# Kernel optimization log

Hardware: AMD Instinct MI355X
Metric: run time of the kernel (lower is better)

Reference implementation:

```python
import jax, jax.numpy as jnp
import numpy as np

D_MODEL, D_STATE, D_CONV, D_INNER = 1024, 16, 4, 2048
BATCH, SEQ = 2, 2048


def setup_inputs() -> dict:
    key = jax.random.key(0)
    ks = jax.random.split(key, 12)
    s = 0.02
    inp = {
        "x": jax.random.normal(ks[0], (BATCH, SEQ, D_MODEL), jnp.float32),
        # Linear weights stored (in, out): y = x @ W + b (equivalent to torch x @ W.T + b)
        "W_in": jax.random.normal(ks[1], (D_MODEL, 2 * D_INNER), jnp.float32) * s,
        "b_in": jnp.zeros((2 * D_INNER,), jnp.float32),
        # depthwise conv kernel (OIH) with groups=d_inner -> (d_inner, 1, d_conv)
        "conv_w": jax.random.normal(ks[2], (D_INNER, 1, D_CONV), jnp.float32) * s,
        "conv_b": jnp.zeros((D_INNER,), jnp.float32),
        "W_x": jax.random.normal(ks[3], (D_INNER, 2 * D_STATE), jnp.float32) * s,
        "b_x": jnp.zeros((2 * D_STATE,), jnp.float32),
        "W_dt": jax.random.normal(ks[4], (D_INNER, D_INNER), jnp.float32) * s,
        "b_dt": jnp.zeros((D_INNER,), jnp.float32),
        # A_log init: log(arange(1..d_state)) tiled over d_inner, as in the module
        "A_log": jnp.log(jnp.tile(jnp.arange(1, D_STATE + 1, dtype=jnp.float32), (D_INNER, 1))),
        "D": jnp.ones((D_INNER,), jnp.float32),
        "W_out": jax.random.normal(ks[5], (D_INNER, D_MODEL), jnp.float32) * s,
        "b_out": jnp.zeros((D_MODEL,), jnp.float32),
    }
    return inp


def reference(x, W_in, b_in, conv_w, conv_b, W_x, b_x, W_dt, b_dt, A_log, D, W_out, b_out):
    d_inner, d_state = A_log.shape
    d_conv = conv_w.shape[-1]
    bsz, seq_len, _ = x.shape

    xz = x @ W_in + b_in                      # (B, L, 2*Din)
    xh, z = jnp.split(xz, 2, axis=-1)

    # causal depthwise conv: torch pads both sides by d_conv-1 then slices [:L]
    # == left-pad-only causal conv
    xc = jnp.transpose(xh, (0, 2, 1))         # (B, Din, L)
    xc = jax.lax.conv_general_dilated(
        xc, conv_w, window_strides=(1,), padding=[(d_conv - 1, 0)],
        dimension_numbers=("NCH", "OIH", "NCH"), feature_group_count=d_inner)
    xc = xc + conv_b[None, :, None]
    xh = jax.nn.silu(jnp.transpose(xc, (0, 2, 1)))  # (B, L, Din)

    A = -jnp.exp(A_log)                       # (Din, N)
    x_dbl = xh @ W_x + b_x                    # (B, L, 2N)
    Bmat = x_dbl[..., d_state:]               # second chunk; first chunk is discarded
    delta = jax.nn.softplus(xh @ W_dt + b_dt) # (B, L, Din)

    def step(h, inp):
        d_t, b_t, u_t = inp                    # (B,Din), (B,N), (B,Din)
        dA = jnp.exp(d_t[:, :, None] * A)      # (B, Din, N)
        dBu = d_t[:, :, None] * b_t[:, None, :] * u_t[:, :, None]
        h = dA * h + dBu
        return h, h.sum(-1)                    # y_t: (B, Din)

    h0 = jnp.zeros((bsz, d_inner, d_state), x.dtype)
    _, ys = jax.lax.scan(step, h0, (jnp.swapaxes(delta, 0, 1),
                                    jnp.swapaxes(Bmat, 0, 1),
                                    jnp.swapaxes(xh, 0, 1)))
    y = jnp.swapaxes(ys, 0, 1) + xh * D       # skip connection with D
    y = y * jax.nn.silu(z)                    # gate
    return y @ W_out + b_out                  # (B, L, d_model)
```

## Files before the change

### kernel.cpp

```cpp
#include <hip/hip_runtime.h>
#include <stdint.h>

#define NDM   1024
#define NDS   16
#define NDC   4
#define NDI   2048
#define NB    2
#define NL    2048
#define MROWS (NB*NL)
#define CCH   32
#define CLEN  64

typedef __bf16 bf16x8 __attribute__((ext_vector_type(8)));
typedef float  f32x4  __attribute__((ext_vector_type(4)));
typedef short  short8 __attribute__((ext_vector_type(8)));

__device__ __forceinline__ short f2bf(float f) {
  union { float f; unsigned u; } x; x.f = f;
  unsigned r = (x.u + 0x7FFFu + ((x.u >> 16) & 1u)) >> 16;
  return (short)r;
}

__device__ __forceinline__ void gload16(const void* g, void* l) {
  __builtin_amdgcn_global_load_lds(
      (__attribute__((address_space(1))) void*)(uintptr_t)g,
      (__attribute__((address_space(3))) void*)l,
      16, 0, 0);
}

__device__ __forceinline__ size_t fgoff(int row, int k8, int K) {
  return (size_t)(row >> 4) * K * 16 + (size_t)k8 * 128 + (row & 15) * 8;
}

__global__ __launch_bounds__(256) void cvt_fg_kernel(
    const float* __restrict__ in, short* __restrict__ out) {
  __shared__ short slab[16][1032];
  const int tid = threadIdx.x;
  const int g = blockIdx.x;
  const float* p = in + (size_t)g * 16 * 1024;
  #pragma unroll
  for (int u = 0; u < 8; ++u) {
    int unit = u * 256 + tid;
    int rr = unit >> 7, cc = unit & 127;
    const float* rp = p + (size_t)rr * 1024 + cc * 8;
    #pragma unroll
    for (int e = 0; e < 8; ++e) slab[rr][cc * 8 + e] = f2bf(rp[e]);
  }
  __syncthreads();
  short* op = out + (size_t)g * 16384;
  #pragma unroll
  for (int u = 0; u < 8; ++u) {
    int u2 = u * 256 + tid;
    int rr = u2 & 15, k8 = u2 >> 4;
    *(short8*)&op[k8 * 128 + rr * 8] = *(short8*)&slab[rr][k8 * 8];
  }
}

__global__ __launch_bounds__(256) void transpose_fg_kernel(
    const float* __restrict__ in, short* __restrict__ out, int K, int N) {
  __shared__ float t[64][33];
  const int tx = threadIdx.x, ty = threadIdx.y;
  const int n0 = blockIdx.x * 32, k0 = blockIdx.y * 64;
  #pragma unroll
  for (int i = 0; i < 64; i += 8)
    t[ty + i][tx] = in[(size_t)(k0 + ty + i) * N + n0 + tx];
  __syncthreads();
  const int n = n0 + tx, k8 = (k0 >> 3) + ty;
  short8 v;
  #pragma unroll
  for (int e = 0; e < 8; ++e) v[e] = f2bf(t[ty * 8 + e][tx]);
  *(short8*)&out[fgoff(n, k8, K)] = v;
}

template<int BN, int EPI>
__global__ __launch_bounds__(256, 4) void gemm_fg_kernel(
    const short* __restrict__ A, const short* __restrict__ Bt,
    const float* __restrict__ bias, float* __restrict__ C,
    int M, int N, int K)
{
  const int tid  = threadIdx.x;
  const int lane = tid & 63;
  const int w    = tid >> 6;
  const int wM   = w >> 1;
  const int wN   = w & 1;
  const int g    = lane >> 4;
  const int r    = lane & 15;

  constexpr int FN = BN / 32;
  constexpr int QB = BN / 64;

  const int bm = blockIdx.y * 128;
  const int bn = blockIdx.x * BN;

  __shared__ short sA[2][4096];
  __shared__ short sB[2][BN * 32];

  f32x4 acc[4][FN];
  #pragma unroll
  for (int m = 0; m < 4; ++m)
    #pragma unroll
    for (int n = 0; n < FN; ++n)
      acc[m][n] = (f32x4){0.f, 0.f, 0.f, 0.f};

  const short* pA[2];
  const short* pB[QB];
  #pragma unroll
  for (int q = 0; q < 2; ++q)
    pA[q] = A + (size_t)((bm >> 4) + w * 2 + q) * K * 16 + lane * 8;
  #pragma unroll
  for (int q = 0; q < QB; ++q)
    pB[q] = Bt + (size_t)((bn >> 4) + w * QB + q) * K * 16 + lane * 8;

#define STAGE(buf, kb)                                                       \
  do {                                                                       \
    _Pragma("unroll")                                                        \
    for (int q = 0; q < 2; ++q)                                              \
      gload16(pA[q] + (size_t)(kb) * 16, &sA[buf][(w * 2 + q) * 512]);       \
    _Pragma("unroll")                                                        \
    for (int q = 0; q < QB; ++q)                                             \
      gload16(pB[q] + (size_t)(kb) * 16, &sB[buf][(w * QB + q) * 512]);      \
  } while (0)

  STAGE(0, 0);
  int cur = 0;
  for (int kb = 0; kb < K; kb += 32) {
    __syncthreads();
    if (kb + 32 < K) STAGE(cur ^ 1, kb + 32);

    bf16x8 af[4], bfv[FN];
    #pragma unroll
    for (int m = 0; m < 4; ++m)
      af[m] = *(const bf16x8*)&sA[cur][(wM * 4 + m) * 512 + lane * 8];
    #pragma unroll
    for (int n = 0; n < FN; ++n)
      bfv[n] = *(const bf16x8*)&sB[cur][(wN * FN + n) * 512 + lane * 8];

    #pragma unroll
    for (int m = 0; m < 4; ++m)
      #pragma unroll
      for (int n = 0; n < FN; ++n)
        acc[m][n] = __builtin_amdgcn_mfma_f32_16x16x32_bf16(
            af[m], bfv[n], acc[m][n], 0, 0, 0);
    cur ^= 1;
  }
#undef STAGE

  #pragma unroll
  for (int m = 0; m < 4; ++m) {
    const int row0 = bm + wM * 64 + m * 16 + g * 4;
    #pragma unroll
    for (int n = 0; n < FN; ++n) {
      const int col = bn + wN * (BN / 2) + n * 16 + r;
      const float bv = bias[col];
      #pragma unroll
      for (int e = 0; e < 4; ++e) {
        float v = acc[m][n][e] + bv;
        if (EPI == 1) v = (v > 15.f) ? v : log1pf(__expf(v));
        C[(size_t)(row0 + e) * N + col] = v;
      }
    }
  }
}

__global__ __launch_bounds__(256) void conv_silu_kernel(
    const float* __restrict__ xz, const float* __restrict__ cw,
    const float* __restrict__ cb, float* __restrict__ xh,
    short* __restrict__ xhbf) {
  __shared__ short slab[16][528];
  const int tid = threadIdx.x;
  const int c0 = blockIdx.x * 512;
  const int r0 = blockIdx.y * 16;
  const int b  = r0 >> 11;
  const int t0 = r0 & (NL - 1);
  const float* zbase = xz + ((size_t)b * NL) * (2 * NDI);

  #pragma unroll
  for (int u = 0; u < 4; ++u) {
    int unit = u * 256 + tid;
    int rr = unit >> 6, cc = unit & 63;
    int t = t0 + rr, c = c0 + cc * 8;
    float acc[8];
    #pragma unroll
    for (int e = 0; e < 8; ++e) acc[e] = cb[c + e];
    #pragma unroll
    for (int k = 0; k < NDC; ++k) {
      int tt = t - (NDC - 1) + k;
      if (tt >= 0) {
        const float* rp = zbase + (size_t)tt * (2 * NDI) + c;
        #pragma unroll
        for (int e = 0; e < 8; ++e) acc[e] += cw[(c + e) * NDC + k] * rp[e];
      }
    }
    float* xo = xh + (size_t)(r0 + rr) * NDI + c;
    #pragma unroll
    for (int e = 0; e < 8; ++e) {
      float s = acc[e] / (1.f + __expf(-acc[e]));
      xo[e] = s;
      slab[rr][cc * 8 + e] = f2bf(s);
    }
  }
  __syncthreads();
  short* op = xhbf + (size_t)(r0 >> 4) * NDI * 16 + (size_t)(c0 >> 3) * 128;
  #pragma unroll
  for (int u = 0; u < 4; ++u) {
    int u2 = u * 256 + tid;
    int rr = u2 & 15, q = u2 >> 4;
    *(short8*)&op[q * 128 + rr * 8] = *(short8*)&slab[rr][q * 8];
  }
}

__global__ __launch_bounds__(256) void bmat_kernel(
    const float* __restrict__ xh, const float* __restrict__ Wx,
    const float* __restrict__ bx, float* __restrict__ Bm) {
  const int row  = blockIdx.x * 4 + (threadIdx.x >> 6);
  const int lane = threadIdx.x & 63;
  const int s = lane & 15, q = lane >> 4;
  const float* xr = xh + (size_t)row * NDI;
  float acc = 0.f;
  for (int c = q * 512; c < (q + 1) * 512; ++c)
    acc += xr[c] * Wx[c * (2 * NDS) + NDS + s];
  acc += __shfl_xor(acc, 16);
  acc += __shfl_xor(acc, 32);
  if (lane < 16) Bm[(size_t)row * NDS + s] = acc + bx[NDS + s];
}

__device__ __forceinline__ size_t scoff(int b, int k, int c) {
  return (((size_t)b * CCH + k) * NDI + c) * NDS;
}

__global__ __launch_bounds__(256) void scan_p1_kernel(
    const float* __restrict__ delta, const float* __restrict__ Bm,
    const float* __restrict__ xh, const float* __restrict__ A_log,
    float* __restrict__ Pbuf, float* __restrict__ Hend) {
  const int i = blockIdx.x * 256 + threadIdx.x;
  const int c = i & (NDI - 1);
  const int k = (i >> 11) & (CCH - 1);
  const int b = i >> 16;
  const int t0 = k * CLEN;

  float Av[NDS];
  #pragma unroll
  for (int s = 0; s < NDS; ++s) Av[s] = -__expf(A_log[c * NDS + s]);

  const float* dp = delta + ((size_t)(b * NL + t0)) * NDI + c;
  const float* up = xh    + ((size_t)(b * NL + t0)) * NDI + c;
  const f32x4* Bp = (const f32x4*)(Bm + ((size_t)(b * NL + t0)) * NDS);

  float h[NDS], P[NDS];
  #pragma unroll
  for (int s = 0; s < NDS; ++s) { h[s] = 0.f; P[s] = 1.f; }

  #pragma unroll 4
  for (int j = 0; j < CLEN; ++j) {
    const float d = dp[(size_t)j * NDI];
    const float u = up[(size_t)j * NDI];
    f32x4 B0 = Bp[j * 4 + 0], B1 = Bp[j * 4 + 1];
    f32x4 B2 = Bp[j * 4 + 2], B3 = Bp[j * 4 + 3];
    const float du = d * u;
    float Bv[NDS];
    #pragma unroll
    for (int e = 0; e < 4; ++e) {
      Bv[e] = B0[e]; Bv[4 + e] = B1[e]; Bv[8 + e] = B2[e]; Bv[12 + e] = B3[e];
    }
    #pragma unroll
    for (int s = 0; s < NDS; ++s) {
      float dA = __expf(d * Av[s]);
      h[s] = dA * h[s] + du * Bv[s];
      P[s] *= dA;
    }
  }

  const size_t base = scoff(b, k, c);
  #pragma unroll
  for (int q = 0; q < 4; ++q) {
    *(f32x4*)&Pbuf[base + q * 4] = (f32x4){P[q*4], P[q*4+1], P[q*4+2], P[q*4+3]};
    *(f32x4*)&Hend[base + q * 4] = (f32x4){h[q*4], h[q*4+1], h[q*4+2], h[q*4+3]};
  }
}

__global__ __launch_bounds__(256) void scan_p2_kernel(
    const float* __restrict__ Pbuf, const float* __restrict__ Hend,
    float* __restrict__ Hin) {
  const int i = blockIdx.x * 256 + threadIdx.x;
  const int s = i & (NDS - 1);
  const int c = (i >> 4) & (NDI - 1);
  const int b = i >> 15;
  const size_t step = (size_t)NDI * NDS;
  const size_t base = scoff(b, 0, c) + s;
  float h = 0.f;
  #pragma unroll 8
  for (int k = 0; k < CCH; ++k) {
    Hin[base + (size_t)k * step] = h;
    h = Hend[base + (size_t)k * step] + Pbuf[base + (size_t)k * step] * h;
  }
}

__global__ __launch_bounds__(256) void scan_p3_kernel(
    const float* __restrict__ delta, const float* __restrict__ Bm,
    const float* __restrict__ xh, const float* __restrict__ A_log,
    const float* __restrict__ Hin, const float* __restrict__ Dvec,
    const float* __restrict__ xz, short* __restrict__ ybf) {
  const int tid = threadIdx.x;
  const int i = blockIdx.x * 256 + tid;
  const int c = i & (NDI - 1);
  const int k = (i >> 11) & (CCH - 1);
  const int b = i >> 16;
  const int t0 = k * CLEN;
  const int cb0 = (blockIdx.x * 256) & (NDI - 1);

  __shared__ float ylds[16][257];

  float Av[NDS];
  #pragma unroll
  for (int s = 0; s < NDS; ++s) Av[s] = -__expf(A_log[c * NDS + s]);
  const float dcoef = Dvec[c];

  const float* dp = delta + ((size_t)(b * NL + t0)) * NDI + c;
  const float* up = xh    + ((size_t)(b * NL + t0)) * NDI + c;
  const f32x4* Bp = (const f32x4*)(Bm + ((size_t)(b * NL + t0)) * NDS);
  const float* zp = xz    + ((size_t)(b * NL + t0)) * (2 * NDI) + NDI + c;

  const size_t base = scoff(b, k, c);
  float h[NDS];
  #pragma unroll
  for (int s = 0; s < NDS; ++s) h[s] = Hin[base + s];

  for (int j = 0; j < CLEN; ++j) {
    const float d = dp[(size_t)j * NDI];
    const float u = up[(size_t)j * NDI];
    f32x4 B0 = Bp[j * 4 + 0], B1 = Bp[j * 4 + 1];
    f32x4 B2 = Bp[j * 4 + 2], B3 = Bp[j * 4 + 3];
    const float du = d * u;
    float Bv[NDS];
    #pragma unroll
    for (int e = 0; e < 4; ++e) {
      Bv[e] = B0[e]; Bv[4 + e] = B1[e]; Bv[8 + e] = B2[e]; Bv[12 + e] = B3[e];
    }
    #pragma unroll
    for (int s = 0; s < NDS; ++s) {
      float dA = __expf(d * Av[s]);
      h[s] = dA * h[s] + du * Bv[s];
    }
    float sum01 = 0.f, sum23 = 0.f;
    #pragma unroll
    for (int s = 0; s < 8; ++s)  sum01 += h[s];
    #pragma unroll
    for (int s = 8; s < 16; ++s) sum23 += h[s];
    float y = sum01 + sum23 + u * dcoef;
    float z = zp[(size_t)j * (2 * NDI)];
    y *= z / (1.f + __expf(-z));
    ylds[j & 15][tid] = y;

    if ((j & 15) == 15) {
      __syncthreads();
      const int jb = j - 15;
      #pragma unroll
      for (int s2 = 0; s2 < 2; ++s2) {
        int u2 = tid + 256 * s2;
        int tt = u2 & 15, q = u2 >> 4;
        short8 v;
        #pragma unroll
        for (int e = 0; e < 8; ++e) v[e] = f2bf(ylds[tt][q * 8 + e]);
        int grow = b * NL + t0 + jb + tt;
        int k8 = (cb0 >> 3) + q;
        *(short8*)&ybf[fgoff(grow, k8, NDI)] = v;
      }
      __syncthreads();
    }
  }
}

extern "C" void kernel_launch(void* const* d_in, const int* in_sizes, int n_in,
                              void* d_out, int out_size, void* d_ws, size_t ws_size,
                              hipStream_t stream) {
  const float* x      = (const float*)d_in[0];
  const float* W_in   = (const float*)d_in[1];
  const float* b_in   = (const float*)d_in[2];
  const float* conv_w = (const float*)d_in[3];
  const float* conv_b = (const float*)d_in[4];
  const float* W_x    = (const float*)d_in[5];
  const float* b_x    = (const float*)d_in[6];
  const float* W_dt   = (const float*)d_in[7];
  const float* b_dt   = (const float*)d_in[8];
  const float* A_log  = (const float*)d_in[9];
  const float* Dv     = (const float*)d_in[10];
  const float* W_out  = (const float*)d_in[11];
  const float* b_out  = (const float*)d_in[12];
  float* out = (float*)d_out;

  char* w = (char*)d_ws;
  short* xbf   = (short*)(w);
  short* WtIn  = (short*)(w + 8388608);
  short* WtDt  = (short*)(w + 16777216);
  short* WtOut = (short*)(w + 25165824);
  float* xz    = (float*)(w + 29360128);
  float* xhf   = (float*)(w + 96468992);
  short* xhbf  = (short*)(w + 130023424);
  float* delta = (float*)(w + 146800640);
  float* Bm    = (float*)(w + 180355072);
  short* ybf   = (short*)(w + 214171648);
  float* Pbuf  = (float*)(w);
  float* Hend  = (float*)(w + 8388608);
  float* Hin   = (float*)(w + 16777216);

  cvt_fg_kernel<<<MROWS / 16, 256, 0, stream>>>(x, xbf);
  transpose_fg_kernel<<<dim3((2 * NDI) / 32, NDM / 64), dim3(32, 8), 0, stream>>>(
      W_in, WtIn, NDM, 2 * NDI);
  transpose_fg_kernel<<<dim3(NDI / 32, NDI / 64), dim3(32, 8), 0, stream>>>(
      W_dt, WtDt, NDI, NDI);
  transpose_fg_kernel<<<dim3(NDM / 32, NDI / 64), dim3(32, 8), 0, stream>>>(
      W_out, WtOut, NDI, NDM);

  gemm_fg_kernel<128, 0><<<dim3((2 * NDI) / 128, MROWS / 128), 256, 0, stream>>>(
      xbf, WtIn, b_in, xz, MROWS, 2 * NDI, NDM);

  conv_silu_kernel<<<dim3(NDI / 512, MROWS / 16), 256, 0, stream>>>(
      xz, conv_w, conv_b, xhf, xhbf);

  bmat_kernel<<<MROWS / 4, 256, 0, stream>>>(xhf, W_x, b_x, Bm);

  gemm_fg_kernel<128, 1><<<dim3(NDI / 128, MROWS / 128), 256, 0, stream>>>(
      xhbf, WtDt, b_dt, delta, MROWS, NDI, NDI);

  scan_p1_kernel<<<(NB * NDI * CCH) / 256, 256, 0, stream>>>(
      delta, Bm, xhf, A_log, Pbuf, Hend);
  scan_p2_kernel<<<(NB * NDI * NDS) / 256, 256, 0, stream>>>(Pbuf, Hend, Hin);
  scan_p3_kernel<<<(NB * NDI * CCH) / 256, 256, 0, stream>>>(
      delta, Bm, xhf, A_log, Hin, Dv, xz, ybf);

  gemm_fg_kernel<64, 0><<<dim3(NDM / 64, MROWS / 128), 256, 0, stream>>>(
      ybf, WtOut, b_out, out, MROWS, NDM, NDI);
}
```

Baseline: 347.1 us.

## Load GEMM fragments directly from global into registers, dropping LDS staging

Result: no change. 347.9 us (+0.2%).

```diff
diff --git a/kernel.cpp b/kernel.cpp
--- a/kernel.cpp
+++ b/kernel.cpp
@@ -21,13 +21,6 @@
   return (short)r;
 }
 
-__device__ __forceinline__ void gload16(const void* g, void* l) {
-  __builtin_amdgcn_global_load_lds(
-      (__attribute__((address_space(1))) void*)(uintptr_t)g,
-      (__attribute__((address_space(3))) void*)l,
-      16, 0, 0);
-}
-
 __device__ __forceinline__ size_t fgoff(int row, int k8, int K) {
   return (size_t)(row >> 4) * K * 16 + (size_t)k8 * 128 + (row & 15) * 8;
 }
@@ -73,7 +66,7 @@
 }
 
 template<int BN, int EPI>
-__global__ __launch_bounds__(256, 4) void gemm_fg_kernel(
+__global__ __launch_bounds__(256, 2) void gemm_fg_kernel(
     const short* __restrict__ A, const short* __restrict__ Bt,
     const float* __restrict__ bias, float* __restrict__ C,
     int M, int N, int K)
@@ -87,13 +80,22 @@
   const int r    = lane & 15;
 
   constexpr int FN = BN / 32;
-  constexpr int QB = BN / 64;
-
-  const int bm = blockIdx.y * 128;
-  const int bn = blockIdx.x * BN;
-
-  __shared__ short sA[2][4096];
-  __shared__ short sB[2][BN * 32];
+
+  const int nx  = gridDim.x;
+  const int nwg = nx * gridDim.y;
+  const int bid = blockIdx.y * nx + blockIdx.x;
+  const int swz = (bid & 7) * (nwg >> 3) + (bid >> 3);
+  const int bm  = (swz / nx) * 128;
+  const int bn  = (swz % nx) * BN;
+
+  const short* pA[4];
+  const short* pB[FN];
+  #pragma unroll
+  for (int m = 0; m < 4; ++m)
+    pA[m] = A + (size_t)((bm >> 4) + wM * 4 + m) * K * 16 + lane * 8;
+  #pragma unroll
+  for (int n = 0; n < FN; ++n)
+    pB[n] = Bt + (size_t)((bn >> 4) + wN * FN + n) * K * 16 + lane * 8;
 
   f32x4 acc[4][FN];
   #pragma unroll
@@ -102,48 +104,43 @@
     for (int n = 0; n < FN; ++n)
       acc[m][n] = (f32x4){0.f, 0.f, 0.f, 0.f};
 
-  const short* pA[2];
-  const short* pB[QB];
-  #pragma unroll
-  for (int q = 0; q < 2; ++q)
-    pA[q] = A + (size_t)((bm >> 4) + w * 2 + q) * K * 16 + lane * 8;
-  #pragma unroll
-  for (int q = 0; q < QB; ++q)
-    pB[q] = Bt + (size_t)((bn >> 4) + w * QB + q) * K * 16 + lane * 8;
-
-#define STAGE(buf, kb)                                                       \
-  do {                                                                       \
-    _Pragma("unroll")                                                        \
-    for (int q = 0; q < 2; ++q)                                              \
-      gload16(pA[q] + (size_t)(kb) * 16, &sA[buf][(w * 2 + q) * 512]);       \
-    _Pragma("unroll")                                                        \
-    for (int q = 0; q < QB; ++q)                                             \
-      gload16(pB[q] + (size_t)(kb) * 16, &sB[buf][(w * QB + q) * 512]);      \
-  } while (0)
-
-  STAGE(0, 0);
-  int cur = 0;
-  for (int kb = 0; kb < K; kb += 32) {
-    __syncthreads();
-    if (kb + 32 < K) STAGE(cur ^ 1, kb + 32);
-
-    bf16x8 af[4], bfv[FN];
-    #pragma unroll
-    for (int m = 0; m < 4; ++m)
-      af[m] = *(const bf16x8*)&sA[cur][(wM * 4 + m) * 512 + lane * 8];
-    #pragma unroll
-    for (int n = 0; n < FN; ++n)
-      bfv[n] = *(const bf16x8*)&sB[cur][(wN * FN + n) * 512 + lane * 8];
-
+  bf16x8 a0[4], b0[FN], a1[4], b1[FN];
+  #pragma unroll
+  for (int m = 0; m < 4; ++m) a0[m] = *(const bf16x8*)(pA[m]);
+  #pragma unroll
+  for (int n = 0; n < FN; ++n) b0[n] = *(const bf16x8*)(pB[n]);
+
+  for (int kb = 0; kb < K; kb += 64) {
+    if (kb + 32 < K) {
+      #pragma unroll
+      for (int m = 0; m < 4; ++m)
+        a1[m] = *(const bf16x8*)(pA[m] + (size_t)(kb + 32) * 16);
+      #pragma unroll
+      for (int n = 0; n < FN; ++n)
+        b1[n] = *(const bf16x8*)(pB[n] + (size_t)(kb + 32) * 16);
+    }
     #pragma unroll
     for (int m = 0; m < 4; ++m)
       #pragma unroll
       for (int n = 0; n < FN; ++n)
         acc[m][n] = __builtin_amdgcn_mfma_f32_16x16x32_bf16(
-            af[m], bfv[n], acc[m][n], 0, 0, 0);
-    cur ^= 1;
-  }
-#undef STAGE
+            a0[m], b0[n], acc[m][n], 0, 0, 0);
+
+    if (kb + 64 < K) {
+      #pragma unroll
+      for (int m = 0; m < 4; ++m)
+        a0[m] = *(const bf16x8*)(pA[m] + (size_t)(kb + 64) * 16);
+      #pragma unroll
+      for (int n = 0; n < FN; ++n)
+        b0[n] = *(const bf16x8*)(pB[n] + (size_t)(kb + 64) * 16);
+    }
+    #pragma unroll
+    for (int m = 0; m < 4; ++m)
+      #pragma unroll
+      for (int n = 0; n < FN; ++n)
+        acc[m][n] = __builtin_amdgcn_mfma_f32_16x16x32_bf16(
+            a1[m], b1[n], acc[m][n], 0, 0, 0);
+  }
 
   #pragma unroll
   for (int m = 0; m < 4; ++m) {
```
